# Optimization experiments

Hardware: AMD Instinct MI355X
Metric: run time of the kernel (lower is better)

The kernel has to match this reference:

```python
import jax, jax.numpy as jnp
import numpy as np

B, S, V, E, P, C = 256, 128, 32000, 300, 200, 3
DIST_CUTOFF = 10

def _seq_mask(x):
    # TF: count_nonzero over seq, sequence_mask, expand to [B, S, 1]
    size = jnp.sum(x != 0, axis=1)
    m = (jnp.arange(S)[None, :] < size[:, None]).astype(jnp.float32)
    return m[:, :, None]

def _l2norm(w):
    n = jnp.sqrt(jnp.maximum(jnp.sum(w * w, axis=-1, keepdims=True), 1e-12))
    return w / n

def setup_inputs() -> dict:
    key = jax.random.key(0)
    ks = jax.random.split(key, 11)
    std = 0.01
    x1 = jax.random.randint(ks[0], (B, S), 0, V, dtype=jnp.int32)
    x2 = jax.random.randint(ks[1], (B, S), 0, V, dtype=jnp.int32)
    emb = jax.random.normal(ks[2], (V, E), jnp.float32)
    w_intra = jax.random.normal(ks[3], (E, E), jnp.float32) * std
    bias_intra = jax.random.normal(ks[4], (1,), jnp.float32) * std
    w_proj1 = jax.random.normal(ks[5], (2 * E, P), jnp.float32) * std
    w_proj2 = jax.random.normal(ks[6], (2 * E, P), jnp.float32) * std
    w_att = jax.random.normal(ks[7], (P, P), jnp.float32) * std
    w_cmp1 = jax.random.normal(ks[8], (2 * P, 2 * P), jnp.float32) * std
    w_cmp2 = jax.random.normal(ks[9], (2 * P, 2 * P), jnp.float32) * std
    w_agg = jax.random.normal(ks[10], (4 * P, C), jnp.float32) * std
    return dict(x1=x1, x2=x2, emb=emb, w_intra=w_intra, bias_intra=bias_intra,
                w_proj1=w_proj1, w_proj2=w_proj2, w_att=w_att,
                w_cmp1=w_cmp1, w_cmp2=w_cmp2, w_agg=w_agg)

def reference(x1, x2, emb, w_intra, bias_intra, w_proj1, w_proj2, w_att, w_cmp1, w_cmp2, w_agg):
    relu = jax.nn.relu
    mask1, mask2 = _seq_mask(x1), _seq_mask(x2)  # [B,S,1]

    # normalized embedding lookup
    e = _l2norm(emb)
    e1, e2 = e[x1], e[x2]  # [B,S,E]

    # intra-attention with distance bias (bias zeroed for |i-j| < 10)
    idx = jnp.arange(S)
    dist = jnp.abs(idx[None, :] - idx[:, None])
    dbias = bias_intra[0] * (dist >= DIST_CUTOFF).astype(jnp.float32)  # [S,S]

    def intra(x):
        f = relu(x @ w_intra)                       # shared F, [B,S,E]
        att = jnp.einsum('bik,bjk->bij', f, f)      # [B,S,S]
        sm = jax.nn.softmax(att + dbias[None], axis=2)
        xp = jnp.einsum('bik,bkj->bij', sm, x)
        return jnp.concatenate([x, xp], axis=2)     # [B,S,2E]

    e1, e2 = intra(e1), intra(e2)

    # project
    x1p = relu(e1 @ w_proj1)  # [B,S,P]
    x2p = relu(e2 @ w_proj2)

    # attend: F(x1) . F(x2), multiplicative mask, two softmaxes
    f1 = relu(x1p @ w_att)
    f2 = relu(x2p @ w_att)
    sim = jnp.einsum('bik,bjk->bij', f1, f2)          # [B,S1,S2]
    sim = sim * (mask1 * jnp.swapaxes(mask2, 1, 2))   # multiplicative mask (as in source)
    alpha = jnp.einsum('bki,bkj->bij', jax.nn.softmax(sim, axis=1), x1p)  # [B,S2,P]
    beta = jnp.einsum('bik,bkj->bij', jax.nn.softmax(sim, axis=2), x2p)   # [B,S1,P]

    # compare
    v1 = relu(jnp.concatenate([x1p, beta], axis=2) @ w_cmp1)
    v2 = relu(jnp.concatenate([x2p, alpha], axis=2) @ w_cmp2)

    # aggregate (masked sum pooling) + final ReLU projection (faithful to source)
    v1 = jnp.sum(v1 * mask1, axis=1)
    v2 = jnp.sum(v2 * mask2, axis=1)
    y_hat = relu(jnp.concatenate([v1, v2], axis=1) @ w_agg)  # [B,C]
    return y_hat
```

## Files before the change

### kernel.cpp

```cpp
#include <hip/hip_runtime.h>

#define BATCH 256
#define SEQ   128
#define EDIM  300
#define PDIM  200
#define BSTOK (BATCH * SEQ)

#define F_RELU  1
#define F_ACCUM 2

typedef unsigned short u16;
typedef __attribute__((ext_vector_type(8))) short bf16x8;
typedef __attribute__((ext_vector_type(4))) float f32x4;

__device__ __forceinline__ u16 f2bf(float x) {
    unsigned u = __float_as_uint(x);
    unsigned r = u + 0x7fffu + ((u >> 16) & 1u);
    return (u16)(r >> 16);
}
__device__ __forceinline__ float bf2f(u16 h) {
    return __uint_as_float(((unsigned)h) << 16);
}

__device__ __forceinline__ void split_store(const float* va, u16* dH, u16* dL)
{
    unsigned hp[8], lp[8];
    #pragma unroll
    for (int i = 0; i < 8; i++) {
        const unsigned u0 = __float_as_uint(va[2 * i]);
        const unsigned u1 = __float_as_uint(va[2 * i + 1]);
        const unsigned h0 = u0 & 0xffff0000u;
        const unsigned h1 = u1 & 0xffff0000u;
        hp[i] = (u0 >> 16) | h1;
        const float r0 = va[2 * i]     - __uint_as_float(h0);
        const float r1 = va[2 * i + 1] - __uint_as_float(h1);
        lp[i] = (__float_as_uint(r0) >> 16) | (__float_as_uint(r1) & 0xffff0000u);
    }
    ((uint4*)dH)[0] = make_uint4(hp[0], hp[1], hp[2], hp[3]);
    ((uint4*)dH)[1] = make_uint4(hp[4], hp[5], hp[6], hp[7]);
    ((uint4*)dL)[0] = make_uint4(lp[0], lp[1], lp[2], lp[3]);
    ((uint4*)dL)[1] = make_uint4(lp[4], lp[5], lp[6], lp[7]);
}

__device__ __forceinline__ void hi_store(const float* va, u16* dH)
{
    unsigned hp[8];
    #pragma unroll
    for (int i = 0; i < 8; i++)
        hp[i] = (unsigned)f2bf(va[2 * i]) | ((unsigned)f2bf(va[2 * i + 1]) << 16);
    ((uint4*)dH)[0] = make_uint4(hp[0], hp[1], hp[2], hp[3]);
    ((uint4*)dH)[1] = make_uint4(hp[4], hp[5], hp[6], hp[7]);
}

__device__ __forceinline__ void load16(float* va, const float* __restrict__ src,
                                       bool row_ok, int kbase, int Kvalid)
{
    if (row_ok) {
        #pragma unroll
        for (int i = 0; i < 4; i++) {
            const float4 v = *(const float4*)(src + i * 4);
            va[i * 4 + 0] = v.x; va[i * 4 + 1] = v.y;
            va[i * 4 + 2] = v.z; va[i * 4 + 3] = v.w;
        }
        #pragma unroll
        for (int i = 0; i < 16; i++)
            va[i] = (kbase + i < Kvalid) ? va[i] : 0.f;
    } else {
        #pragma unroll
        for (int i = 0; i < 16; i++) va[i] = 0.f;
    }
}

__device__ __forceinline__ void stage16(const float* __restrict__ src, bool row_ok,
                                        int kbase, int Kvalid, u16* dH, u16* dL)
{
    float va[16];
    load16(va, src, row_ok, kbase, Kvalid);
    split_store(va, dH, dL);
}

__device__ __forceinline__ void stage16_hi(const float* __restrict__ src, bool row_ok,
                                           int kbase, int Kvalid, u16* dH)
{
    float va[16];
    load16(va, src, row_ok, kbase, Kvalid);
    hi_store(va, dH);
}

__device__ __forceinline__ void gather16(float* va, const float* __restrict__ erow,
                                         float nrm, int kb)
{
    if (kb + 16 <= EDIM) {
        #pragma unroll
        for (int i = 0; i < 4; i++) {
            const float4 v = *(const float4*)(erow + kb + i * 4);
            va[i * 4 + 0] = v.x; va[i * 4 + 1] = v.y;
            va[i * 4 + 2] = v.z; va[i * 4 + 3] = v.w;
        }
    } else {
        #pragma unroll
        for (int i = 0; i < 16; i++)
            va[i] = (kb + i < EDIM) ? erow[kb + i] : 0.f;
    }
    #pragma unroll
    for (int i = 0; i < 16; i++) va[i] *= nrm;
}

__device__ __forceinline__ void stage_gather(const float* __restrict__ erow, float nrm,
                                             int kb, u16* dH, u16* dL)
{
    float va[16];
    gather16(va, erow, nrm, kb);
    split_store(va, dH, dL);
}

__device__ __forceinline__ void stage_gather_hi(const float* __restrict__ erow, float nrm,
                                                int kb, u16* dH)
{
    float va[16];
    gather16(va, erow, nrm, kb);
    hi_store(va, dH);
}

#define MFMA3(ai, aj) \
    acc[ai][aj] = __builtin_amdgcn_mfma_f32_16x16x32_bf16(fah[ai], fbh[aj], acc[ai][aj], 0, 0, 0); \
    acc[ai][aj] = __builtin_amdgcn_mfma_f32_16x16x32_bf16(fah[ai], fbl[aj], acc[ai][aj], 0, 0, 0); \
    acc[ai][aj] = __builtin_amdgcn_mfma_f32_16x16x32_bf16(fal[ai], fbh[aj], acc[ai][aj], 0, 0, 0);

#define MFMA1(ai, aj) \
    acc[ai][aj] = __builtin_amdgcn_mfma_f32_16x16x32_bf16(fah[ai], fbh[aj], acc[ai][aj], 0, 0, 0);

__device__ __forceinline__ void store_transposed(
    float* __restrict__ PT, const f32x4 (*acc)[4], float* TR,
    int bn, int Nvalid, int wm, int wn, int lr, int quad, int tid, bool relu)
{
    #pragma unroll
    for (int h = 0; h < 2; h++) {
        __syncthreads();
        if ((wn >> 6) == h) {
            #pragma unroll
            for (int j = 0; j < 4; j++) {
                const int col = j * 16 + lr;
                #pragma unroll
                for (int i = 0; i < 4; i++)
                    #pragma unroll
                    for (int r = 0; r < 4; r++) {
                        float v = acc[i][j][r];
                        if (relu) v = fmaxf(v, 0.f);
                        TR[col * 129 + wm + i * 16 + quad * 4 + r] = v;
                    }
            }
        }
        __syncthreads();
        const int row = tid >> 2;
        const int gp = bn + h * 64 + row;
        if (gp < Nvalid) {
            float* dst = PT + (long long)gp * 128;
            for (int c = (tid & 3); c < 32; c += 4) {
                const int base = row * 129 + c * 4;
                *(float4*)(dst + c * 4) =
                    make_float4(TR[base], TR[base + 1], TR[base + 2], TR[base + 3]);
            }
        }
    }
}

__global__ __launch_bounds__(256) void gemm_proj(
    const int* __restrict__ x1, const int* __restrict__ x2,
    const float* __restrict__ emb, const float* __restrict__ norms,
    const u16* __restrict__ W1h, const u16* __restrict__ W1l,
    const u16* __restrict__ W2h, const u16* __restrict__ W2l,
    float* __restrict__ T, float* __restrict__ F0, float* __restrict__ F1)
{
    __shared__ __align__(16) unsigned char smem[40960];
    u16 (*AsH)[40] = (u16(*)[40])(smem);
    u16 (*AsL)[40] = (u16(*)[40])(smem + 10240);
    u16 (*BsH)[40] = (u16(*)[40])(smem + 20480);
    u16 (*BsL)[40] = (u16(*)[40])(smem + 30720);

    const int tid = threadIdx.x;
    const int id  = blockIdx.y * 5 + blockIdx.x;
    const int xcd = id & 7;
    const int s   = id >> 3;
    const int mt  = xcd + 8 * (s / 5);
    const int bm  = mt * 128;
    const int bn  = (s % 5) * 128;
    const bool side2 = mt >= 256;
    const bool wb = bn < 256;

    const u16* Bh = side2 ? W2h : W1h;
    const u16* Bl = side2 ? W2l : W1l;
    float* F = side2 ? F1 : F0;
    const int fm = side2 ? bm - 32768 : bm;
    const int* toks = (side2 ? x2 - 32768 : x1) + bm;

    const int wave = tid >> 6;
    const int lane = tid & 63;
    const int wm   = (wave >> 1) * 64;
    const int wn   = (wave & 1) * 64;
    const int lr   = lane & 15;
    const int quad = lane >> 4;
    const int sr   = tid >> 1;
    const int sc   = (tid & 1) * 16;

    const int tok = toks[sr];
    const float nrm = norms[tok];
    const float* erow = emb + (long long)tok * EDIM;

    f32x4 acc[4][4];
    #pragma unroll
    for (int i = 0; i < 4; i++)
        #pragma unroll
        for (int j = 0; j < 4; j++)
            acc[i][j] = (f32x4)(0.0f);

    for (int k0 = 0; k0 < 320; k0 += 32) {
        if (wb) stage_gather(erow, nrm, k0 + sc, &AsH[sr][sc], &AsL[sr][sc]);
        else    stage_gather_hi(erow, nrm, k0 + sc, &AsH[sr][sc]);
        {
            uint4 wh0 = make_uint4(0,0,0,0), wh1 = make_uint4(0,0,0,0);
            const int gn = bn + sr;
            const long long br = (long long)gn * 320 + k0 + sc;
            if (gn < 556) {
                wh0 = *(const uint4*)(Bh + br);
                wh1 = *(const uint4*)(Bh + br + 8);
            }
            *(uint4*)&BsH[sr][sc]     = wh0;
            *(uint4*)&BsH[sr][sc + 8] = wh1;
            if (wb) {
                uint4 wl0 = make_uint4(0,0,0,0), wl1 = make_uint4(0,0,0,0);
                if (gn < 556) {
                    wl0 = *(const uint4*)(Bl + br);
                    wl1 = *(const uint4*)(Bl + br + 8);
                }
                *(uint4*)&BsL[sr][sc]     = wl0;
                *(uint4*)&BsL[sr][sc + 8] = wl1;
            }
        }
        __syncthreads();

        bf16x8 fah[4], fal[4], fbh[4], fbl[4];
        #pragma unroll
        for (int i = 0; i < 4; i++) {
            fah[i] = *(const bf16x8*)&AsH[wm + i * 16 + lr][quad * 8];
            fbh[i] = *(const bf16x8*)&BsH[wn + i * 16 + lr][quad * 8];
        }
        if (wb) {
            #pragma unroll
            for (int i = 0; i < 4; i++) {
                fal[i] = *(const bf16x8*)&AsL[wm + i * 16 + lr][quad * 8];
                fbl[i] = *(const bf16x8*)&BsL[wn + i * 16 + lr][quad * 8];
            }
            #pragma unroll
            for (int i = 0; i < 4; i++)
                #pragma unroll
                for (int j = 0; j < 4; j++) { MFMA3(i, j) }
        } else {
            #pragma unroll
            for (int i = 0; i < 4; i++)
                #pragma unroll
                for (int j = 0; j < 4; j++) { MFMA1(i, j) }
        }
        __syncthreads();
    }

    if (wb) {
        float* Tb = T + (long long)mt * (PDIM * SEQ);
        store_transposed(Tb, acc, (float*)smem, bn, PDIM, wm, wn, lr, quad, tid, false);
    } else {
        #pragma unroll
        for (int i = 0; i < 4; i++) {
            #pragma unroll
            for (int j = 0; j < 4; j++) {
                const int idx = bn + wn + j * 16 + lr - 256;
                if (idx >= EDIM) continue;
                #pragma unroll
                for (int r = 0; r < 4; r++) {
                    const int gm = fm + wm + i * 16 + quad * 4 + r;
                    F[(long long)gm * EDIM + idx] = fmaxf(acc[i][j][r], 0.f);
                }
            }
        }
    }
}

__global__ __launch_bounds__(256) void gemm_xp(
    const float* __restrict__ P, float* __restrict__ T,
    const int* __restrict__ x1, const int* __restrict__ x2,
    const float* __restrict__ emb, const float* __restrict__ norms,
    const u16* __restrict__ W1h, const u16* __restrict__ W1l,
    const u16* __restrict__ W2h, const u16* __restrict__ W2l,
    float* __restrict__ XCAT)
{
    __shared__ __align__(16) unsigned char smem[40960];
    u16 (*AsH)[40] = (u16(*)[40])(smem);
    u16 (*AsL)[40] = (u16(*)[40])(smem + 10240);
    u16 (*BsH)[40] = (u16(*)[40])(smem + 20480);
    u16 (*BsL)[40] = (u16(*)[40])(smem + 30720);

    const int tid = threadIdx.x;
    const int bz  = blockIdx.z;
    const int bn  = blockIdx.x * 128;

    const int wave = tid >> 6;
    const int lane = tid & 63;
    const int wm   = (wave >> 1) * 64;
    const int wn   = (wave & 1) * 64;
    const int lr   = lane & 15;
    const int quad = lane >> 4;
    const int sr   = tid >> 1;
    const int sc   = (tid & 1) * 16;

    const int* toks = (bz < BATCH) ? x1 + bz * SEQ : x2 + (bz - BATCH) * SEQ;
    const u16* Wh = (bz < BATCH) ? W1h : W2h;
    const u16* Wl = (bz < BATCH) ? W1l : W2l;
    const int tok = toks[sr];
    const float nrm = norms[tok];
    const float* erow = emb + (long long)tok * EDIM;
    const float* Pb = P + (long long)bz * (SEQ * SEQ);
    float* Tb = T + (long long)bz * (PDIM * SEQ);

    f32x4 acc[4][4];
    #pragma unroll
    for (int i = 0; i < 4; i++)
        #pragma unroll
        for (int j = 0; j < 4; j++)
            acc[i][j] = (f32x4)(0.0f);

    for (int k0 = 0; k0 < 320; k0 += 32) {
        stage_gather(erow, nrm, k0 + sc, &AsH[sr][sc], &AsL[sr][sc]);
        {
            uint4 wh0 = make_uint4(0,0,0,0), wh1 = make_uint4(0,0,0,0);
            uint4 wl0 = make_uint4(0,0,0,0), wl1 = make_uint4(0,0,0,0);
            const int gn = bn + sr;
            if (gn < PDIM) {
                const long long br = (long long)gn * 320 + k0 + sc;
                wh0 = *(const uint4*)(Wh + br);
                wh1 = *(const uint4*)(Wh + br + 8);
                wl0 = *(const uint4*)(Wl + br);
                wl1 = *(const uint4*)(Wl + br + 8);
            }
            *(uint4*)&BsH[sr][sc]     = wh0;
            *(uint4*)&BsH[sr][sc + 8] = wh1;
            *(uint4*)&BsL[sr][sc]     = wl0;
            *(uint4*)&BsL[sr][sc + 8] = wl1;
        }
        __syncthreads();

        bf16x8 fah[4], fal[4], fbh[4], fbl[4];
        #pragma unroll
        for (int i = 0; i < 4; i++) {
            fah[i] = *(const bf16x8*)&AsH[wm + i * 16 + lr][quad * 8];
            fal[i] = *(const bf16x8*)&AsL[wm + i * 16 + lr][quad * 8];
            fbh[i] = *(const bf16x8*)&BsH[wn + i * 16 + lr][quad * 8];
            fbl[i] = *(const bf16x8*)&BsL[wn + i * 16 + lr][quad * 8];
        }
        #pragma unroll
        for (int i = 0; i < 4; i++)
            #pragma unroll
            for (int j = 0; j < 4; j++) { MFMA3(i, j) }
        __syncthreads();
    }

    for (int k0 = 0; k0 < 128; k0 += 32) {
        stage16(Pb + (long long)sr * 128 + k0 + sc, true, 0, 1 << 30,
                &AsH[sr][sc], &AsL[sr][sc]);
        const int gn = bn + sr;
        stage16(Tb + (long long)gn * 128 + k0 + sc, gn < PDIM, 0, 1 << 30,
                &BsH[sr][sc], &BsL[sr][sc]);
        __syncthreads();

        bf16x8 fah[4], fal[4], fbh[4], fbl[4];
        #pragma unroll
        for (int i = 0; i < 4; i++) {
            fah[i] = *(const bf16x8*)&AsH[wm + i * 16 + lr][quad * 8];
            fal[i] = *(const bf16x8*)&AsL[wm + i * 16 + lr][quad * 8];
            fbh[i] = *(const bf16x8*)&BsH[wn + i * 16 + lr][quad * 8];
            fbl[i] = *(const bf16x8*)&BsL[wn + i * 16 + lr][quad * 8];
        }
        #pragma unroll
        for (int i = 0; i < 4; i++)
            #pragma unroll
            for (int j = 0; j < 4; j++) { MFMA3(i, j) }
        __syncthreads();
    }

    const long long rowbase = (long long)bz * SEQ;
    #pragma unroll
    for (int i = 0; i < 4; i++) {
        #pragma unroll
        for (int j = 0; j < 4; j++) {
            const int gn = bn + wn + j * 16 + lr;
            if (gn >= PDIM) continue;
            #pragma unroll
            for (int r = 0; r < 4; r++) {
                const int gm = wm + i * 16 + quad * 4 + r;
                XCAT[(rowbase + gm) * 400 + gn] = fmaxf(acc[i][j][r], 0.f);
            }
        }
    }
    store_transposed(Tb, acc, (float*)smem, bn, PDIM, wm, wn, lr, quad, tid, true);
}

template <int NM>
__global__ __launch_bounds__(256) void gemm_flat(
    const float* __restrict__ A,
    const u16* __restrict__ Bh, const u16* __restrict__ Bl,
    const u16* __restrict__ Bh2, const u16* __restrict__ Bl2, int Msplit,
    float* __restrict__ C, float* __restrict__ PO, const int* __restrict__ sizes,
    int M, int N, int Kp, int lda, int ldb, int ldc, int flags)
{
    __shared__ u16 AsH[128][40];
    __shared__ u16 AsL[128][40];
    __shared__ u16 BsH[128][40];
    __shared__ u16 BsL[128][40];

    const int tid = threadIdx.x;
    int bx = blockIdx.x, by = blockIdx.y;
    if ((gridDim.y & 7) == 0) {
        const int gx = gridDim.x;
        const int id = by * gx + bx;
        const int xcd = id & 7;
        const int s = id >> 3;
        by = xcd + 8 * (s / gx);
        bx = s % gx;
    }
    const int bm = by * 128;
    const int bn = bx * 128;

    const int wave = tid >> 6;
    const int lane = tid & 63;
    const int wm   = (wave >> 1) * 64;
    const int wn   = (wave & 1) * 64;
    const int lr   = lane & 15;
    const int quad = lane >> 4;
    const int sr   = tid >> 1;
    const int sc   = (tid & 1) * 16;

    if (bm >= Msplit) { Bh = Bh2; Bl = Bl2; }

    f32x4 acc[4][4];
    #pragma unroll
    for (int i = 0; i < 4; i++)
        #pragma unroll
        for (int j = 0; j < 4; j++)
            acc[i][j] = (f32x4)(0.0f);

    for (int k0 = 0; k0 < Kp; k0 += 32) {
        if constexpr (NM == 3)
            stage16(A + (long long)(bm + sr) * lda + k0 + sc, true, 0, 1 << 30,
                    &AsH[sr][sc], &AsL[sr][sc]);
        else
            stage16_hi(A + (long long)(bm + sr) * lda + k0 + sc, true, 0, 1 << 30,
                       &AsH[sr][sc]);
        {
            uint4 wh0 = make_uint4(0,0,0,0), wh1 = make_uint4(0,0,0,0);
            const int gn = bn + sr;
            const long long br = (long long)gn * ldb + k0 + sc;
            if (gn < N) {
                wh0 = *(const uint4*)(Bh + br);
                wh1 = *(const uint4*)(Bh + br + 8);
            }
            *(uint4*)&BsH[sr][sc]     = wh0;
            *(uint4*)&BsH[sr][sc + 8] = wh1;
            if constexpr (NM == 3) {
                uint4 wl0 = make_uint4(0,0,0,0), wl1 = make_uint4(0,0,0,0);
                if (gn < N) {
                    wl0 = *(const uint4*)(Bl + br);
                    wl1 = *(const uint4*)(Bl + br + 8);
                }
                *(uint4*)&BsL[sr][sc]     = wl0;
                *(uint4*)&BsL[sr][sc + 8] = wl1;
            }
        }
        __syncthreads();

        bf16x8 fah[4], fal[4], fbh[4], fbl[4];
        #pragma unroll
        for (int i = 0; i < 4; i++) {
            fah[i] = *(const bf16x8*)&AsH[wm + i * 16 + lr][quad * 8];
            fbh[i] = *(const bf16x8*)&BsH[wn + i * 16 + lr][quad * 8];
        }
        if constexpr (NM == 3) {
            #pragma unroll
            for (int i = 0; i < 4; i++) {
                fal[i] = *(const bf16x8*)&AsL[wm + i * 16 + lr][quad * 8];
                fbl[i] = *(const bf16x8*)&BsL[wn + i * 16 + lr][quad * 8];
            }
            #pragma unroll
            for (int i = 0; i < 4; i++)
                #pragma unroll
                for (int j = 0; j < 4; j++) { MFMA3(i, j) }
        } else {
            #pragma unroll
            for (int i = 0; i < 4; i++)
                #pragma unroll
                for (int j = 0; j < 4; j++) { MFMA1(i, j) }
        }
        __syncthreads();
    }

    const int sz = PO ? sizes[bm >> 7] : 0;
    float ps[4] = {0.f, 0.f, 0.f, 0.f};
    #pragma unroll
    for (int j = 0; j < 4; j++) {
        const int gn = bn + wn + j * 16 + lr;
        const bool gok = gn < N;
        #pragma unroll
        for (int i = 0; i < 4; i++) {
            #pragma unroll
            for (int r = 0; r < 4; r++) {
                const int row = wm + i * 16 + quad * 4 + r;
                const int gm = bm + row;
                float v = acc[i][j][r];
                if (flags & F_RELU) v = fmaxf(v, 0.f);
                if (gok && C) C[(long long)gm * ldc + gn] = v;
                if (PO && row < sz) ps[j] += v;
            }
        }
    }
    if (PO) {
        #pragma unroll
        for (int j = 0; j < 4; j++) {
            ps[j] += __shfl_xor(ps[j], 16);
            ps[j] += __shfl_xor(ps[j], 32);
        }
        float* PS = (float*)AsH;
        if (wm == 0 && quad == 0) {
            #pragma unroll
            for (int j = 0; j < 4; j++) PS[wn + j * 16 + lr] = ps[j];
        }
        __syncthreads();
        if (wm == 64 && quad == 0) {
            #pragma unroll
            for (int j = 0; j < 4; j++) PS[wn + j * 16 + lr] += ps[j];
        }
        __syncthreads();
        if (tid < 128) {
            const int gn = bn + tid;
            if (gn < N) PO[(long long)(bm >> 7) * N + gn] = PS[tid];
        }
    }
}

template <int MODE>
__global__ __launch_bounds__(256) void gemm_bat(
    const float* __restrict__ A, const float* __restrict__ Aalt,
    const float* __restrict__ B, const float* __restrict__ Balt,
    float* __restrict__ C, float* __restrict__ PT,
    int N, int Kvalid, int Kp, int lda, int ldb, int ldc,
    long long sA, long long sB, long long sC, long long sPT,
    int flags, const float* __restrict__ bias_ptr, const int* __restrict__ sizes,
    int same_ab)
{
    constexpr int NM = (MODE == 0) ? 3 : 1;
    constexpr int SB = (MODE >= 1) ? 65536 : 40960;
    __shared__ __align__(16) unsigned char smem[SB];
    u16 (*AsH)[40] = (u16(*)[40])(smem);
    u16 (*AsL)[40] = (u16(*)[40])(smem + 10240);
    u16 (*BsH)[40] = (u16(*)[40])(smem + 20480);
    u16 (*BsL)[40] = (u16(*)[40])(smem + 30720);

    const int bz = blockIdx.z;
    long long zb = bz;
    const float* Ause = A;
    const float* Buse = B;
    if (Aalt && bz >= BATCH) { Ause = Aalt; Buse = Balt; zb = bz - BATCH; }
    Ause += zb * sA;
    Buse += zb * sB;
    C += (long long)bz * sC;
    if (PT) PT += (long long)bz * sPT;

    const int tid  = threadIdx.x;
    const int bn   = blockIdx.x * 128;
    const int wave = tid >> 6;
    const int lane = tid & 63;
    const int wm   = (wave >> 1) * 64;
    const int wn   = (wave & 1) * 64;
    const int lr   = lane & 15;
    const int quad = lane >> 4;
    const int sr   = tid >> 1;
    const int sc   = (tid & 1) * 16;

    f32x4 acc[4][4];
    #pragma unroll
    for (int i = 0; i < 4; i++)
        #pragma unroll
        for (int j = 0; j < 4; j++)
            acc[i][j] = (f32x4)(0.0f);

    u16 (*fbH)[40] = same_ab ? AsH : BsH;
    u16 (*fbL)[40] = same_ab ? AsL : BsL;

    for (int k0 = 0; k0 < Kp; k0 += 32) {
        if constexpr (NM == 3)
            stage16(Ause + (long long)sr * lda + k0 + sc, true, k0 + sc, Kvalid,
                    &AsH[sr][sc], &AsL[sr][sc]);
        else
            stage16_hi(Ause + (long long)sr * lda + k0 + sc, true, k0 + sc, Kvalid,
                       &AsH[sr][sc]);
        if (!same_ab) {
            const int gn = bn + sr;
            if constexpr (NM == 3)
                stage16(Buse + (long long)gn * ldb + k0 + sc, gn < N, k0 + sc, Kvalid,
                        &BsH[sr][sc], &BsL[sr][sc]);
            else
                stage16_hi(Buse + (long long)gn * ldb + k0 + sc, gn < N, k0 + sc, Kvalid,
                           &BsH[sr][sc]);
        }
        __syncthreads();

        bf16x8 fah[4], fal[4], fbh[4], fbl[4];
        #pragma unroll
        for (int i = 0; i < 4; i++) {
            fah[i] = *(const bf16x8*)&AsH[wm + i * 16 + lr][quad * 8];
            fbh[i] = *(const bf16x8*)&fbH[wn + i * 16 + lr][quad * 8];
        }
        if constexpr (NM == 3) {
            #pragma unroll
            for (int i = 0; i < 4; i++) {
                fal[i] = *(const bf16x8*)&AsL[wm + i * 16 + lr][quad * 8];
                fbl[i] = *(const bf16x8*)&fbL[wn + i * 16 + lr][quad * 8];
            }
            #pragma unroll
            for (int i = 0; i < 4; i++)
                #pragma unroll
                for (int j = 0; j < 4; j++) { MFMA3(i, j) }
        } else {
            #pragma unroll
            for (int i = 0; i < 4; i++)
                #pragma unroll
                for (int j = 0; j < 4; j++) { MFMA1(i, j) }
        }
        __syncthreads();
    }

    if (MODE == 1) {
        float* S = (float*)smem;
        const float bias = bias_ptr[0];
        #pragma unroll
        for (int i = 0; i < 4; i++) {
            #pragma unroll
            for (int j = 0; j < 4; j++) {
                const int col = wn + j * 16 + lr;
                #pragma unroll
                for (int r = 0; r < 4; r++) {
                    const int row = wm + i * 16 + quad * 4 + r;
                    int d = row - col; d = d < 0 ? -d : d;
                    S[row * 128 + col] = acc[i][j][r] + ((d >= 10) ? bias : 0.f);
                }
            }
        }
        __syncthreads();
        const int row = tid >> 1;
        const int half = (tid & 1) * 64;
        float mx = -1e30f;
        for (int c = 0; c < 64; c++) mx = fmaxf(mx, S[row * 128 + half + c]);
        mx = fmaxf(mx, __shfl_xor(mx, 1));
        float sum = 0.f;
        for (int c = 0; c < 64; c++) sum += __expf(S[row * 128 + half + c] - mx);
        sum += __shfl_xor(sum, 1);
        const float inv = 1.f / sum;
        for (int c = 0; c < 64; c++)
            C[(long long)row * ldc + half + c] = __expf(S[row * 128 + half + c] - mx) * inv;
    } else if (MODE == 2) {
        float* S = (float*)smem;
        const int s1 = sizes[bz];
        const int s2 = sizes[BATCH + bz];
        #pragma unroll
        for (int i = 0; i < 4; i++) {
            #pragma unroll
            for (int j = 0; j < 4; j++) {
                const int col = wn + j * 16 + lr;
                #pragma unroll
                for (int r = 0; r < 4; r++) {
                    const int row = wm + i * 16 + quad * 4 + r;
                    float v = acc[i][j][r];
                    if (row >= s1 || col >= s2) v = 0.f;
                    S[row * 128 + col] = v;
                }
            }
        }
        __syncthreads();
        const int idx = tid >> 1;
        const int half = (tid & 1) * 64;
        {
            float mx = -1e30f;
            for (int c = 0; c < 64; c++) mx = fmaxf(mx, S[idx * 128 + half + c]);
            mx = fmaxf(mx, __shfl_xor(mx, 1));
            float sum = 0.f;
            for (int c = 0; c < 64; c++) sum += __expf(S[idx * 128 + half + c] - mx);
            sum += __shfl_xor(sum, 1);
            const float inv = 1.f / sum;
            for (int c = 0; c < 64; c++)
                C[(long long)idx * 128 + half + c] = __expf(S[idx * 128 + half + c] - mx) * inv;
        }
        {
            float mx = -1e30f;
            for (int r = 0; r < 64; r++) mx = fmaxf(mx, S[(half + r) * 128 + idx]);
            mx = fmaxf(mx, __shfl_xor(mx, 1));
            float sum = 0.f;
            for (int r = 0; r < 64; r++) sum += __expf(S[(half + r) * 128 + idx] - mx);
            sum += __shfl_xor(sum, 1);
            const float inv = 1.f / sum;
            for (int r = 0; r < 64; r++)
                PT[(long long)idx * 128 + half + r] = __expf(S[(half + r) * 128 + idx] - mx) * inv;
        }
    } else {
        const int s1 = sizes ? sizes[bz] : SEQ;
        const int s2 = sizes ? sizes[BATCH + bz] : SEQ;
        #pragma unroll
        for (int i = 0; i < 4; i++) {
            #pragma unroll
            for (int j = 0; j < 4; j++) {
                const int gn = bn + wn + j * 16 + lr;
                if (gn >= N) continue;
                #pragma unroll
                for (int r = 0; r < 4; r++) {
                    const int gm = wm + i * 16 + quad * 4 + r;
                    float v = acc[i][j][r];
                    if (sizes && (gm >= s1 || gn >= s2)) v = 0.f;
                    if (flags & F_ACCUM) v += C[(long long)gm * ldc + gn];
                    if (flags & F_RELU)  v = fmaxf(v, 0.f);
                    C[(long long)gm * ldc + gn] = v;
                    if (PT) PT[(long long)gn * 128 + gm] = v;
                }
            }
        }
    }
}

struct WEnt { const float* src; u16* H; u16* L; int K, N, Kp, rowStart; };
struct WTab { WEnt e[11]; };
__global__ void convert_all(WTab t)
{
    const int row = blockIdx.y;
    const int k = blockIdx.x * 256 + threadIdx.x;
    #pragma unroll
    for (int s = 0; s < 11; s++) {
        const WEnt w = t.e[s];
        if (row >= w.rowStart && row < w.rowStart + w.N) {
            const int n = row - w.rowStart;
            if (k < w.Kp) {
                const float v = (k < w.K) ? w.src[(long long)k * w.N + n] : 0.f;
                const u16 h = f2bf(v);
                w.H[(long long)n * w.Kp + k] = h;
                w.L[(long long)n * w.Kp + k] = f2bf(v - bf2f(h));
            }
            return;
        }
    }
}

__global__ void norms_kernel(const float* __restrict__ emb, float* __restrict__ norms)
{
    const int r = blockIdx.x;
    const int lane = threadIdx.x;
    const float* row = emb + (long long)r * EDIM;
    float ss = 0.f;
    #pragma unroll
    for (int i = 0; i < 5; i++) {
        const int c = lane + i * 64;
        const float f = (c < EDIM) ? row[c] : 0.f;
        ss += f * f;
    }
    #pragma unroll
    for (int o = 32; o > 0; o >>= 1) ss += __shfl_xor(ss, o);
    if (lane == 0) norms[r] = rsqrtf(fmaxf(ss, 1e-12f));
}

__global__ void sizes_kernel(const int* __restrict__ x1, const int* __restrict__ x2,
                             int* __restrict__ sizes)
{
    const int b = blockIdx.x;
    const int side = blockIdx.y;
    const int* x = (side ? x2 : x1) + b * SEQ;
    const int nz = (x[threadIdx.x] != 0) ? 1 : 0;
    const unsigned long long bal = __ballot(nz);
    __shared__ int part[2];
    if ((threadIdx.x & 63) == 0) part[threadIdx.x >> 6] = __popcll(bal);
    __syncthreads();
    if (threadIdx.x == 0) sizes[side * BATCH + b] = part[0] + part[1];
}

__global__ void agg_kernel(const float* __restrict__ v1s, const float* __restrict__ v2s,
                           const float* __restrict__ w_agg, float* __restrict__ y)
{
    const int b = blockIdx.x;
    const int lane = threadIdx.x;
    float a0 = 0.f, a1 = 0.f, a2 = 0.f;
    for (int k = lane; k < 800; k += 64) {
        const float v = (k < 400) ? v1s[b * 400 + k] : v2s[b * 400 + k - 400];
        a0 = fmaf(v, w_agg[k * 3 + 0], a0);
        a1 = fmaf(v, w_agg[k * 3 + 1], a1);
        a2 = fmaf(v, w_agg[k * 3 + 2], a2);
    }
    #pragma unroll
    for (int o = 32; o > 0; o >>= 1) {
        a0 += __shfl_xor(a0, o);
        a1 += __shfl_xor(a1, o);
        a2 += __shfl_xor(a2, o);
    }
    if (lane == 0) {
        y[b * 3 + 0] = fmaxf(a0, 0.f);
        y[b * 3 + 1] = fmaxf(a1, 0.f);
        y[b * 3 + 2] = fmaxf(a2, 0.f);
    }
}

extern "C" void kernel_launch(void* const* d_in, const int* in_sizes, int n_in,
                              void* d_out, int out_size, void* d_ws, size_t ws_size,
                              hipStream_t stream)
{
    (void)in_sizes; (void)n_in; (void)out_size; (void)ws_size;
    const int*   x1         = (const int*)d_in[0];
    const int*   x2         = (const int*)d_in[1];
    const float* emb        = (const float*)d_in[2];
    const float* w_intra    = (const float*)d_in[3];
    const float* bias_intra = (const float*)d_in[4];
    const float* w_proj1    = (const float*)d_in[5];
    const float* w_proj2    = (const float*)d_in[6];
    const float* w_att      = (const float*)d_in[7];
    const float* w_cmp1     = (const float*)d_in[8];
    const float* w_cmp2     = (const float*)d_in[9];
    const float* w_agg      = (const float*)d_in[10];
    float* y  = (float*)d_out;
    float* ws = (float*)d_ws;

    float* X1CAT = ws;
    float* X2CAT = X1CAT + 13107200;
    float* T     = X2CAT + 13107200;
    float* FBUF  = T + 13107200;
    float* ATT   = FBUF + 9830400;
    float* POOL  = ATT + 8388608;
    int*   SIZES = (int*)(POOL + 204800);
    float* NORMS = (float*)(SIZES + 512);
    u16*   W1H   = (u16*)(NORMS + 32768);
    u16*   W1L   = W1H + 177920;
    u16*   W2H   = W1L + 177920;
    u16*   W2L   = W2H + 177920;
    u16*   WAH   = W2L + 177920;
    u16*   WAL   = WAH + 44800;
    u16*   WC1H  = WAL + 44800;
    u16*   WC1L  = WC1H + 166400;
    u16*   WC2H  = WC1L + 166400;
    u16*   WC2L  = WC2H + 166400;
    u16*   WPA1H = WC2L + 166400;
    u16*   WPA1L = WPA1H + 64000;
    u16*   WPA2H = WPA1L + 64000;
    u16*   WPA2L = WPA2H + 64000;

    float* F1X = X1CAT;
    float* F12 = FBUF;
    float* F2  = FBUF + 6553600;
    float* SIMP = F2;
    float* SMTP = F12;
    float* T1  = T;
    float* T2  = T + 6553600;

    const long long sbSS = (long long)SEQ * SEQ;
    const long long sbF  = (long long)SEQ * EDIM;
    const long long sbFP = 25600;
    const long long sbC  = (long long)SEQ * 400;
    const long long sbT  = (long long)PDIM * SEQ;

    sizes_kernel<<<dim3(BATCH, 2), 128, 0, stream>>>(x1, x2, SIZES);
    norms_kernel<<<32000, 64, 0, stream>>>(emb, NORMS);

    {
        WTab t;
        t.e[0]  = { w_proj1 + 300 * 200, W1H,             W1L,             300, 200, 320, 0    };
        t.e[1]  = { w_intra,             W1H + 200 * 320, W1L + 200 * 320,   0,  56, 320, 200  };
        t.e[2]  = { w_intra,             W1H + 256 * 320, W1L + 256 * 320, 300, 300, 320, 256  };
        t.e[3]  = { w_proj2 + 300 * 200, W2H,             W2L,             300, 200, 320, 556  };
        t.e[4]  = { w_intra,             W2H + 200 * 320, W2L + 200 * 320,   0,  56, 320, 756  };
        t.e[5]  = { w_intra,             W2H + 256 * 320, W2L + 256 * 320, 300, 300, 320, 812  };
        t.e[6]  = { w_att,               WAH,             WAL,             200, 200, 224, 1112 };
        t.e[7]  = { w_cmp1,              WC1H,            WC1L,            400, 400, 416, 1312 };
        t.e[8]  = { w_cmp2,              WC2H,            WC2L,            400, 400, 416, 1712 };
        t.e[9]  = { w_proj1,             WPA1H,           WPA1L,           300, 200, 320, 2112 };
        t.e[10] = { w_proj2,             WPA2H,           WPA2L,           300, 200, 320, 2312 };
        convert_all<<<dim3(2, 2512), 256, 0, stream>>>(t);
    }

    gemm_proj<<<dim3(5, 512), 256, 0, stream>>>(
        x1, x2, emb, NORMS, W1H, W1L, W2H, W2L, T, FBUF, F1X);
    gemm_bat<1><<<dim3(1, 1, 2 * BATCH), 256, 0, stream>>>(
        FBUF, F1X, FBUF, nullptr, ATT, nullptr,
        SEQ, EDIM, 320, EDIM, EDIM, SEQ, sbF, sbF, sbSS, 0,
        0, bias_intra, nullptr, 1);
    gemm_xp<<<dim3(2, 1, 2 * BATCH), 256, 0, stream>>>(
        ATT, T, x1, x2, emb, NORMS, WPA1H, WPA1L, WPA2H, WPA2L, X1CAT);

    gemm_flat<1><<<dim3(2, 512), 256, 0, stream>>>(
        X1CAT, WAH, WAL, WAH, WAL, 1 << 30, F12, nullptr, nullptr,
        2 * BSTOK, PDIM, 224, 400, 224, PDIM, F_RELU);
    gemm_bat<2><<<dim3(1, 1, BATCH), 256, 0, stream>>>(
        F12, nullptr, F2, nullptr, SIMP, SMTP,
        SEQ, PDIM, 224, PDIM, PDIM, SEQ, sbFP, sbFP, sbFP, sbFP,
        0, nullptr, SIZES, 0);
    gemm_bat<0><<<dim3(2, 1, 2 * BATCH), 256, 0, stream>>>(
        SIMP, SMTP, T2, T1, X1CAT + 200, nullptr,
        PDIM, SEQ, SEQ, SEQ, SEQ, 400, sbFP, sbT, sbC, 0,
        0, nullptr, nullptr, 0);

    gemm_flat<3><<<dim3(4, 512), 256, 0, stream>>>(
        X1CAT, WC1H, WC1L, WC2H, WC2L, BSTOK,
        nullptr, POOL, SIZES,
        2 * BSTOK, 400, 416, 400, 416, 400, F_RELU);
    agg_kernel<<<BATCH, 64, 0, stream>>>(POOL, POOL + 102400, w_agg, y);
}
```

Baseline: 550.4 us.

## Register-prefetch next K-tile global loads across all GEMM kernels

```diff
diff --git a/kernel.cpp b/kernel.cpp
--- a/kernel.cpp
+++ b/kernel.cpp
@@ -52,8 +52,8 @@
     ((uint4*)dH)[1] = make_uint4(hp[4], hp[5], hp[6], hp[7]);
 }
 
-__device__ __forceinline__ void load16(float* va, const float* __restrict__ src,
-                                       bool row_ok, int kbase, int Kvalid)
+__device__ __forceinline__ void gload16(float* va, const float* __restrict__ src,
+                                        bool row_ok)
 {
     if (row_ok) {
         #pragma unroll
@@ -62,33 +62,21 @@
             va[i * 4 + 0] = v.x; va[i * 4 + 1] = v.y;
             va[i * 4 + 2] = v.z; va[i * 4 + 3] = v.w;
         }
-        #pragma unroll
-        for (int i = 0; i < 16; i++)
-            va[i] = (kbase + i < Kvalid) ? va[i] : 0.f;
     } else {
         #pragma unroll
         for (int i = 0; i < 16; i++) va[i] = 0.f;
     }
 }
 
-__device__ __forceinline__ void stage16(const float* __restrict__ src, bool row_ok,
-                                        int kbase, int Kvalid, u16* dH, u16* dL)
-{
-    float va[16];
-    load16(va, src, row_ok, kbase, Kvalid);
-    split_store(va, dH, dL);
-}
-
-__device__ __forceinline__ void stage16_hi(const float* __restrict__ src, bool row_ok,
-                                           int kbase, int Kvalid, u16* dH)
-{
-    float va[16];
-    load16(va, src, row_ok, kbase, Kvalid);
-    hi_store(va, dH);
-}
-
-__device__ __forceinline__ void gather16(float* va, const float* __restrict__ erow,
-                                         float nrm, int kb)
+__device__ __forceinline__ void kmask16(float* va, int kbase, int Kvalid)
+{
+    #pragma unroll
+    for (int i = 0; i < 16; i++)
+        va[i] = (kbase + i < Kvalid) ? va[i] : 0.f;
+}
+
+__device__ __forceinline__ void gload_emb(float* va, const float* __restrict__ erow,
+                                          int kb)
 {
     if (kb + 16 <= EDIM) {
         #pragma unroll
@@ -102,23 +90,20 @@
         for (int i = 0; i < 16; i++)
             va[i] = (kb + i < EDIM) ? erow[kb + i] : 0.f;
     }
+}
+
+__device__ __forceinline__ void commit_scale_split(float* va, float nrm,
+                                                   u16* dH, u16* dL)
+{
     #pragma unroll
     for (int i = 0; i < 16; i++) va[i] *= nrm;
-}
-
-__device__ __forceinline__ void stage_gather(const float* __restrict__ erow, float nrm,
-                                             int kb, u16* dH, u16* dL)
-{
-    float va[16];
-    gather16(va, erow, nrm, kb);
     split_store(va, dH, dL);
 }
 
-__device__ __forceinline__ void stage_gather_hi(const float* __restrict__ erow, float nrm,
-                                                int kb, u16* dH)
-{
-    float va[16];
-    gather16(va, erow, nrm, kb);
+__device__ __forceinline__ void commit_scale_hi(float* va, float nrm, u16* dH)
+{
+    #pragma unroll
+    for (int i = 0; i < 16; i++) va[i] *= nrm;
     hi_store(va, dH);
 }
 
@@ -207,6 +192,11 @@
     const float nrm = norms[tok];
     const float* erow = emb + (long long)tok * EDIM;
 
+    const int gn = bn + sr;
+    const bool bok = gn < 556;
+    const u16* Bhp = Bh + (long long)gn * 320 + sc;
+    const u16* Blp = Bl + (long long)gn * 320 + sc;
+
     f32x4 acc[4][4];
     #pragma unroll
     for (int i = 0; i < 4; i++)
@@ -214,27 +204,32 @@
         for (int j = 0; j < 4; j++)
             acc[i][j] = (f32x4)(0.0f);
 
+    float av[16];
+    uint4 bh0, bh1, bl0, bl1;
+    gload_emb(av, erow, sc);
+    bh0 = bok ? *(const uint4*)(Bhp)     : make_uint4(0,0,0,0);
+    bh1 = bok ? *(const uint4*)(Bhp + 8) : make_uint4(0,0,0,0);
+    if (wb) {
+        bl0 = bok ? *(const uint4*)(Blp)     : make_uint4(0,0,0,0);
+        bl1 = bok ? *(const uint4*)(Blp + 8) : make_uint4(0,0,0,0);
+    }
+
     for (int k0 = 0; k0 < 320; k0 += 32) {
-        if (wb) stage_gather(erow, nrm, k0 + sc, &AsH[sr][sc], &AsL[sr][sc]);
-        else    stage_gather_hi(erow, nrm, k0 + sc, &AsH[sr][sc]);
-        {
-            uint4 wh0 = make_uint4(0,0,0,0), wh1 = make_uint4(0,0,0,0);
-            const int gn = bn + sr;
-            const long long br = (long long)gn * 320 + k0 + sc;
-            if (gn < 556) {
-                wh0 = *(const uint4*)(Bh + br);
-                wh1 = *(const uint4*)(Bh + br + 8);
-            }
-            *(uint4*)&BsH[sr][sc]     = wh0;
-            *(uint4*)&BsH[sr][sc + 8] = wh1;
+        if (wb) commit_scale_split(av, nrm, &AsH[sr][sc], &AsL[sr][sc]);
+        else    commit_scale_hi(av, nrm, &AsH[sr][sc]);
+        *(uint4*)&BsH[sr][sc]     = bh0;
+        *(uint4*)&BsH[sr][sc + 8] = bh1;
+        if (wb) {
+            *(uint4*)&BsL[sr][sc]     = bl0;
+            *(uint4*)&BsL[sr][sc + 8] = bl1;
+        }
+        if (k0 + 32 < 320) {
+            gload_emb(av, erow, k0 + 32 + sc);
+            bh0 = bok ? *(const uint4*)(Bhp + k0 + 32)     : make_uint4(0,0,0,0);
+            bh1 = bok ? *(const uint4*)(Bhp + k0 + 40)     : make_uint4(0,0,0,0);
             if (wb) {
-                uint4 wl0 = make_uint4(0,0,0,0), wl1 = make_uint4(0,0,0,0);
-                if (gn < 556) {
-                    wl0 = *(const uint4*)(Bl + br);
-                    wl1 = *(const uint4*)(Bl + br + 8);
-                }
-                *(uint4*)&BsL[sr][sc]     = wl0;
-                *(uint4*)&BsL[sr][sc + 8] = wl1;
+                bl0 = bok ? *(const uint4*)(Blp + k0 + 32) : make_uint4(0,0,0,0);
+                bl1 = bok ? *(const uint4*)(Blp + k0 + 40) : make_uint4(0,0,0,0);
             }
         }
         __syncthreads();
@@ -320,6 +315,13 @@
     const float* Pb = P + (long long)bz * (SEQ * SEQ);
     float* Tb = T + (long long)bz * (PDIM * SEQ);
 
+    const int gn = bn + sr;
+    const bool bok = gn < PDIM;
+    const u16* Whp = Wh + (long long)gn * 320 + sc;
+    const u16* Wlp = Wl + (long long)gn * 320 + sc;
+    const float* Pp = Pb + (long long)sr * 128 + sc;
+    const float* Tp = Tb + (long long)gn * 128 + sc;
+
     f32x4 acc[4][4];
     #pragma unroll
     for (int i = 0; i < 4; i++)
@@ -327,23 +329,29 @@
         for (int j = 0; j < 4; j++)
             acc[i][j] = (f32x4)(0.0f);
 
+    float av[16], bv[16];
+    uint4 bh0, bh1, bl0, bl1;
+    gload_emb(av, erow, sc);
+    bh0 = bok ? *(const uint4*)(Whp)     : make_uint4(0,0,0,0);
+    bh1 = bok ? *(const uint4*)(Whp + 8) : make_uint4(0,0,0,0);
+    bl0 = bok ? *(const uint4*)(Wlp)     : make_uint4(0,0,0,0);
+    bl1 = bok ? *(const uint4*)(Wlp + 8) : make_uint4(0,0,0,0);
+
     for (int k0 = 0; k0 < 320; k0 += 32) {
-        stage_gather(erow, nrm, k0 + sc, &AsH[sr][sc], &AsL[sr][sc]);
-        {
-            uint4 wh0 = make_uint4(0,0,0,0), wh1 = make_uint4(0,0,0,0);
-            uint4 wl0 = make_uint4(0,0,0,0), wl1 = make_uint4(0,0,0,0);
-            const int gn = bn + sr;
-            if (gn < PDIM) {
-                const long long br = (long long)gn * 320 + k0 + sc;
-                wh0 = *(const uint4*)(Wh + br);
-                wh1 = *(const uint4*)(Wh + br + 8);
-                wl0 = *(const uint4*)(Wl + br);
-                wl1 = *(const uint4*)(Wl + br + 8);
-            }
-            *(uint4*)&BsH[sr][sc]     = wh0;
-            *(uint4*)&BsH[sr][sc + 8] = wh1;
-            *(uint4*)&BsL[sr][sc]     = wl0;
-            *(uint4*)&BsL[sr][sc + 8] = wl1;
+        commit_scale_split(av, nrm, &AsH[sr][sc], &AsL[sr][sc]);
+        *(uint4*)&BsH[sr][sc]     = bh0;
+        *(uint4*)&BsH[sr][sc + 8] = bh1;
+        *(uint4*)&BsL[sr][sc]     = bl0;
+        *(uint4*)&BsL[sr][sc + 8] = bl1;
+        if (k0 + 32 < 320) {
+            gload_emb(av, erow, k0 + 32 + sc);
+            bh0 = bok ? *(const uint4*)(Whp + k0 + 32) : make_uint4(0,0,0,0);
+            bh1 = bok ? *(const uint4*)(Whp + k0 + 40) : make_uint4(0,0,0,0);
+            bl0 = bok ? *(const uint4*)(Wlp + k0 + 32) : make_uint4(0,0,0,0);
+            bl1 = bok ? *(const uint4*)(Wlp + k0 + 40) : make_uint4(0,0,0,0);
+        } else {
+            gload16(av, Pp, true);
+            gload16(bv, Tp, bok);
         }
         __syncthreads();
 
@@ -363,11 +371,12 @@
     }
 
     for (int k0 = 0; k0 < 128; k0 += 32) {
-        stage16(Pb + (long long)sr * 128 + k0 + sc, true, 0, 1 << 30,
-                &AsH[sr][sc], &AsL[sr][sc]);
-        const int gn = bn + sr;
-        stage16(Tb + (long long)gn * 128 + k0 + sc, gn < PDIM, 0, 1 << 30,
-                &BsH[sr][sc], &BsL[sr][sc]);
+        split_store(av, &AsH[sr][sc], &AsL[sr][sc]);
+        split_store(bv, &BsH[sr][sc], &BsL[sr][sc]);
+        if (k0 + 32 < 128) {
+            gload16(av, Pp + k0 + 32, true);
+            gload16(bv, Tp + k0 + 32, bok);
+        }
         __syncthreads();
 
         bf16x8 fah[4], fal[4], fbh[4], fbl[4];
@@ -390,12 +399,12 @@
     for (int i = 0; i < 4; i++) {
         #pragma unroll
         for (int j = 0; j < 4; j++) {
-            const int gn = bn + wn + j * 16 + lr;
-            if (gn >= PDIM) continue;
+            const int gnn = bn + wn + j * 16 + lr;
+            if (gnn >= PDIM) continue;
             #pragma unroll
             for (int r = 0; r < 4; r++) {
                 const int gm = wm + i * 16 + quad * 4 + r;
-                XCAT[(rowbase + gm) * 400 + gn] = fmaxf(acc[i][j][r], 0.f);
+                XCAT[(rowbase + gm) * 400 + gnn] = fmaxf(acc[i][j][r], 0.f);
             }
         }
     }
@@ -439,6 +448,12 @@
 
     if (bm >= Msplit) { Bh = Bh2; Bl = Bl2; }
 
+    const float* Ap = A + (long long)(bm + sr) * lda + sc;
+    const int gn = bn + sr;
+    const bool bok = gn < N;
+    const u16* Bhp = Bh + (long long)gn * ldb + sc;
+    const u16* Blp = Bl + (long long)gn * ldb + sc;
+
     f32x4 acc[4][4];
     #pragma unroll
     for (int i = 0; i < 4; i++)
@@ -446,31 +461,32 @@
         for (int j = 0; j < 4; j++)
             acc[i][j] = (f32x4)(0.0f);
 
+    float av[16];
+    uint4 bh0, bh1, bl0, bl1;
+    gload16(av, Ap, true);
+    bh0 = bok ? *(const uint4*)(Bhp)     : make_uint4(0,0,0,0);
+    bh1 = bok ? *(const uint4*)(Bhp + 8) : make_uint4(0,0,0,0);
+    if constexpr (NM == 3) {
+        bl0 = bok ? *(const uint4*)(Blp)     : make_uint4(0,0,0,0);
+        bl1 = bok ? *(const uint4*)(Blp + 8) : make_uint4(0,0,0,0);
+    }
+
     for (int k0 = 0; k0 < Kp; k0 += 32) {
-        if constexpr (NM == 3)
-            stage16(A + (long long)(bm + sr) * lda + k0 + sc, true, 0, 1 << 30,
-                    &AsH[sr][sc], &AsL[sr][sc]);
-        else
-            stage16_hi(A + (long long)(bm + sr) * lda + k0 + sc, true, 0, 1 << 30,
-                       &AsH[sr][sc]);
-        {
-            uint4 wh0 = make_uint4(0,0,0,0), wh1 = make_uint4(0,0,0,0);
-            const int gn = bn + sr;
-            const long long br = (long long)gn * ldb + k0 + sc;
-            if (gn < N) {
-                wh0 = *(const uint4*)(Bh + br);
-                wh1 = *(const uint4*)(Bh + br + 8);
-            }
-            *(uint4*)&BsH[sr][sc]     = wh0;
-            *(uint4*)&BsH[sr][sc + 8] = wh1;
+        if constexpr (NM == 3) split_store(av, &AsH[sr][sc], &AsL[sr][sc]);
+        else                   hi_store(av, &AsH[sr][sc]);
+        *(uint4*)&BsH[sr][sc]     = bh0;
+        *(uint4*)&BsH[sr][sc + 8] = bh1;
+        if constexpr (NM == 3) {
+            *(uint4*)&BsL[sr][sc]     = bl0;
+            *(uint4*)&BsL[sr][sc + 8] = bl1;
+        }
+        if (k0 + 32 < Kp) {
+            gload16(av, Ap + k0 + 32, true);
+            bh0 = bok ? *(const uint4*)(Bhp + k0 + 32) : make_uint4(0,0,0,0);
+            bh1 = bok ? *(const uint4*)(Bhp + k0 + 40) : make_uint4(0,0,0,0);
             if constexpr (NM == 3) {
-                uint4 wl0 = make_uint4(0,0,0,0), wl1 = make_uint4(0,0,0,0);
-                if (gn < N) {
-                    wl0 = *(const uint4*)(Bl + br);
-                    wl1 = *(const uint4*)(Bl + br + 8);
-                }
-                *(uint4*)&BsL[sr][sc]     = wl0;
-                *(uint4*)&BsL[sr][sc + 8] = wl1;
+                bl0 = bok ? *(const uint4*)(Blp + k0 + 32) : make_uint4(0,0,0,0);
+                bl1 = bok ? *(const uint4*)(Blp + k0 + 40) : make_uint4(0,0,0,0);
             }
         }
         __syncthreads();
@@ -504,8 +520,8 @@
     float ps[4] = {0.f, 0.f, 0.f, 0.f};
     #pragma unroll
     for (int j = 0; j < 4; j++) {
-        const int gn = bn + wn + j * 16 + lr;
-        const bool gok = gn < N;
+        const int gnn = bn + wn + j * 16 + lr;
+        const bool gok = gnn < N;
         #pragma unroll
         for (int i = 0; i < 4; i++) {
             #pragma unroll
@@ -514,7 +530,7 @@
                 const int gm = bm + row;
                 float v = acc[i][j][r];
                 if (flags & F_RELU) v = fmaxf(v, 0.f);
-                if (gok && C) C[(long long)gm * ldc + gn] = v;
+                if (gok && C) C[(long long)gm * ldc + gnn] = v;
                 if (PO && row < sz) ps[j] += v;
             }
         }
@@ -537,8 +553,8 @@
         }
         __syncthreads();
         if (tid < 128) {
-            const int gn = bn + tid;
-            if (gn < N) PO[(long long)(bm >> 7) * N + gn] = PS[tid];
+            const int gnn = bn + tid;
+            if (gnn < N) PO[(long long)(bm >> 7) * N + gnn] = PS[tid];
         }
     }
 }
@@ -592,21 +608,27 @@
     u16 (*fbH)[40] = same_ab ? AsH : BsH;
     u16 (*fbL)[40] = same_ab ? AsL : BsL;
 
+    const float* Apt = Ause + (long long)sr * lda + sc;
+    const int gn = bn + sr;
+    const bool bok = gn < N;
+    const float* Bpt = Buse + (long long)gn * ldb + sc;
+
+    float av[16], bv[16];
+    gload16(av, Apt, true);
+    if (!same_ab) gload16(bv, Bpt, bok);
+
     for (int k0 = 0; k0 < Kp; k0 += 32) {
-        if constexpr (NM == 3)
-            stage16(Ause + (long long)sr * lda + k0 + sc, true, k0 + sc, Kvalid,
-                    &AsH[sr][sc], &AsL[sr][sc]);
-        else
-            stage16_hi(Ause + (long long)sr * lda + k0 + sc, true, k0 + sc, Kvalid,
-                       &AsH[sr][sc]);
+        kmask16(av, k0 + sc, Kvalid);
+        if constexpr (NM == 3) split_store(av, &AsH[sr][sc], &AsL[sr][sc]);
+        else                   hi_store(av, &AsH[sr][sc]);
         if (!same_ab) {
-            const int gn = bn + sr;
-            if constexpr (NM == 3)
-                stage16(Buse + (long long)gn * ldb + k0 + sc, gn < N, k0 + sc, Kvalid,
-                        &BsH[sr][sc], &BsL[sr][sc]);
-            else
-                stage16_hi(Buse + (long long)gn * ldb + k0 + sc, gn < N, k0 + sc, Kvalid,
-                           &BsH[sr][sc]);
+            kmask16(bv, k0 + sc, Kvalid);
+            if constexpr (NM == 3) split_store(bv, &BsH[sr][sc], &BsL[sr][sc]);
+            else                   hi_store(bv, &BsH[sr][sc]);
+        }
+        if (k0 + 32 < Kp) {
+            gload16(av, Apt + k0 + 32, true);
+            if (!same_ab) gload16(bv, Bpt + k0 + 32, bok);
         }
         __syncthreads();
 
@@ -713,17 +735,17 @@
         for (int i = 0; i < 4; i++) {
             #pragma unroll
             for (int j = 0; j < 4; j++) {
-                const int gn = bn + wn + j * 16 + lr;
-                if (gn >= N) continue;
+                const int gnn = bn + wn + j * 16 + lr;
+                if (gnn >= N) continue;
                 #pragma unroll
                 for (int r = 0; r < 4; r++) {
                     const int gm = wm + i * 16 + quad * 4 + r;
                     float v = acc[i][j][r];
-                    if (sizes && (gm >= s1 || gn >= s2)) v = 0.f;
-                    if (flags & F_ACCUM) v += C[(long long)gm * ldc + gn];
+                    if (sizes && (gm >= s1 || gnn >= s2)) v = 0.f;
+                    if (flags & F_ACCUM) v += C[(long long)gm * ldc + gnn];
                     if (flags & F_RELU)  v = fmaxf(v, 0.f);
-                    C[(long long)gm * ldc + gn] = v;
-                    if (PT) PT[(long long)gn * 128 + gm] = v;
+                    C[(long long)gm * ldc + gnn] = v;
+                    if (PT) PT[(long long)gnn * 128 + gm] = v;
                 }
             }
         }
```

Result: no change. 557.2 us (+1.2%).
